# Kernel optimization log

Measured on AMD Instinct MI355X. Metric: run time of the kernel, lower is better.

Reference implementation:

```python
import jax, jax.numpy as jnp
import numpy as np

B, S, D, N, K = 2, 2048, 512, 32768, 64
CHUNK = 2048  # min(2048, num_slots) as in the torch source
EPS = 1e-8


def _phase_linear(x, Wr, Wi, br, bi):
    # complex linear on [..., d, 2] phase tensors
    xr, xi = x[..., 0], x[..., 1]
    yr = xr @ Wr.T - xi @ Wi.T + br
    yi = xr @ Wi.T + xi @ Wr.T + bi
    return jnp.stack([yr, yi], axis=-1)


def _phase_norm(x, gamma):
    # RMS normalization of the complex magnitude over dim, scaled by gamma
    mag2 = (x * x).sum(-1)                      # [..., d]
    rms = jnp.sqrt(mag2.mean(-1, keepdims=True) + EPS)
    return x * (gamma / rms)[..., None]


def setup_inputs() -> dict:
    key = jax.random.key(0)
    ks = jax.random.split(key, 8)
    inp = {
        'query': jax.random.normal(ks[0], (B, S, D, 2), jnp.float32),
        'keys': jax.random.normal(ks[1], (N, D, 2), jnp.float32) * 0.02,
        'values': jax.random.normal(ks[2], (N, D, 2), jnp.float32) * 0.02,
        'Wq_r': jax.random.normal(ks[3], (D, D), jnp.float32) * 0.02,
        'Wq_i': jax.random.normal(ks[4], (D, D), jnp.float32) * 0.02,
        'bq_r': jnp.zeros((D,), jnp.float32),
        'bq_i': jnp.zeros((D,), jnp.float32),
        'Wo_r': jax.random.normal(ks[5], (D, D), jnp.float32) * 0.02,
        'Wo_i': jax.random.normal(ks[6], (D, D), jnp.float32) * 0.02,
        'bo_r': jnp.zeros((D,), jnp.float32),
        'bo_i': jnp.zeros((D,), jnp.float32),
        'ln_gamma': jnp.ones((D,), jnp.float32),
        'top_k': K,
    }
    return inp


def _read(query, keys, values, Wq_r, Wq_i, bq_r, bq_i, Wo_r, Wo_i, bo_r, bo_i, ln_gamma, top_k):
    b, s, d, _ = query.shape
    n = keys.shape[0]
    q = _phase_linear(query, Wq_r, Wq_i, bq_r, bq_i)
    qf = q.reshape(b * s, d, 2)
    q_r, q_i = qf[..., 0], qf[..., 1]
    q_mag = jnp.sqrt((q_r * q_r + q_i * q_i).sum(-1) + EPS)  # [Q]
    nq = b * s

    n_chunks = n // CHUNK
    key_chunks = keys.reshape(n_chunks, CHUNK, d, 2)
    offsets = jnp.arange(n_chunks, dtype=jnp.int32) * CHUNK
    local_idx = jnp.arange(CHUNK, dtype=jnp.int32)

    def body(carry, xs):
        tv, ti = carry                      # [Q, K], [Q, K]
        ck, off = xs                        # [C, d, 2], scalar
        k_r, k_i = ck[..., 0], ck[..., 1]
        k_mag = jnp.sqrt((k_r * k_r + k_i * k_i).sum(-1) + EPS)   # [C]
        coh = q_r @ k_r.T + q_i @ k_i.T                            # [Q, C]
        coh = coh / (q_mag[:, None] * k_mag[None, :] + EPS)
        idx = jnp.broadcast_to(off + local_idx, (nq, CHUNK))
        cv = jnp.concatenate([tv, coh], axis=-1)
        ci = jnp.concatenate([ti, idx], axis=-1)
        nv, loc = jax.lax.top_k(cv, top_k)
        ni = jnp.take_along_axis(ci, loc, axis=-1)
        return (nv, ni), None

    init = (jnp.full((nq, top_k), -jnp.inf, jnp.float32),
            jnp.zeros((nq, top_k), jnp.int32))
    (topk_vals, topk_idx), _ = jax.lax.scan(body, init, (key_chunks, offsets))

    attn = jax.nn.softmax(topk_vals, axis=-1)                      # [Q, K]
    gathered = values[topk_idx]                                    # [Q, K, d, 2]
    retrieved = jnp.einsum('qk,qkdp->qdp', attn, gathered).reshape(b, s, d, 2)

    out = _phase_norm(retrieved, ln_gamma)
    out = _phase_linear(out, Wo_r, Wo_i, bo_r, bo_i)
    return out


def reference(query, keys, values, Wq_r, Wq_i, bq_r, bq_i, Wo_r, Wo_i, bo_r, bo_i, ln_gamma, top_k):
    return _read(query, keys, values, Wq_r, Wq_i, bq_r, bq_i, Wo_r, Wo_i, bo_r, bo_i, ln_gamma, top_k)
```

## Files before the change

### kernel.cpp

```cpp
#include <hip/hip_runtime.h>
#include <math.h>
#include <float.h>

#define EPSF 1e-8f
#define EPSD 1e-8
#define D_DIM 512
#define T_DIM 1024
#define K_TOP 64
#define K_KEEP 128
#define NBIN 2048
#define CAND_SORT 1024

typedef __bf16 bf16_t;
typedef __bf16 bf16x8 __attribute__((ext_vector_type(8)));
typedef __bf16 bf16x4 __attribute__((ext_vector_type(4)));
typedef float f32x4 __attribute__((ext_vector_type(4)));

__global__ __launch_bounds__(256)
void rownorm_convert_q_kernel(const double* __restrict__ X, double* __restrict__ magd,
                              bf16_t* __restrict__ Qn, int rows) {
  int r = blockIdx.x;
  if (r >= rows) return;
  int tid = threadIdx.x;
  const double* xr = X + (size_t)r * T_DIM;
  double v[4];
  double s = 0.0;
  #pragma unroll
  for (int i = 0; i < 4; i++) { v[i] = xr[tid * 4 + i]; s += v[i] * v[i]; }
  for (int o = 32; o > 0; o >>= 1) s += __shfl_down(s, o, 64);
  __shared__ double red[4];
  __shared__ double mag_s;
  if ((tid & 63) == 0) red[tid >> 6] = s;
  __syncthreads();
  if (tid == 0) {
    double m = sqrt(red[0] + red[1] + red[2] + red[3] + EPSD);
    magd[r] = m; mag_s = m;
  }
  __syncthreads();
  double inv = 1.0 / mag_s;
  bf16x4 o;
  #pragma unroll
  for (int i = 0; i < 4; i++) o[i] = (bf16_t)((float)(v[i] * inv));
  *(bf16x4*)(Qn + (size_t)r * T_DIM + tid * 4) = o;
}

__global__ __launch_bounds__(256)
void rownorm_convert_k_kernel(const float* __restrict__ X, double* __restrict__ magd,
                              bf16_t* __restrict__ Kn, int rows) {
  int r = blockIdx.x;
  if (r >= rows) return;
  int tid = threadIdx.x;
  float4 v = ((const float4*)(X + (size_t)r * T_DIM))[tid];
  double s = (double)v.x * v.x + (double)v.y * v.y + (double)v.z * v.z + (double)v.w * v.w;
  for (int o = 32; o > 0; o >>= 1) s += __shfl_down(s, o, 64);
  __shared__ double red[4];
  __shared__ float inv_s;
  if ((tid & 63) == 0) red[tid >> 6] = s;
  __syncthreads();
  if (tid == 0) {
    double m = sqrt(red[0] + red[1] + red[2] + red[3] + EPSD);
    magd[r] = m; inv_s = (float)(1.0 / m);
  }
  __syncthreads();
  float inv = inv_s;
  bf16x4 o;
  o[0] = (bf16_t)(v.x * inv); o[1] = (bf16_t)(v.y * inv);
  o[2] = (bf16_t)(v.z * inv); o[3] = (bf16_t)(v.w * inv);
  *(bf16x4*)(Kn + (size_t)r * T_DIM + tid * 4) = o;
}

__global__ __launch_bounds__(256)
void cgemm_f64_kernel(const float* __restrict__ X,
                      const float* __restrict__ Wr, const float* __restrict__ Wi,
                      const float* __restrict__ br, const float* __restrict__ bi,
                      double* __restrict__ Yd, int M) {
  __shared__ float Ar[16][64], Ai[16][64], Br_[16][64], Bi_[16][64];
  int tid = threadIdx.x;
  int tx = tid & 15, ty = tid >> 4;
  int m0 = blockIdx.x * 64, n0 = blockIdx.y * 64;
  double accR[4][4] = {{0}}, accI[4][4] = {{0}};
  for (int k0 = 0; k0 < D_DIM; k0 += 16) {
    #pragma unroll
    for (int gi = 0; gi < 2; gi++) {
      int g = tid + gi * 256;
      int m = g >> 3, dg = g & 7;
      float4 v = *(const float4*)(X + (size_t)(m0 + m) * T_DIM + 2 * k0 + dg * 4);
      Ar[dg*2][m] = v.x; Ai[dg*2][m] = v.y; Ar[dg*2+1][m] = v.z; Ai[dg*2+1][m] = v.w;
    }
    {
      int j = tid >> 2, c = tid & 3;
      float4 vr = *(const float4*)(Wr + (size_t)(n0 + j) * D_DIM + k0 + c * 4);
      float4 vi = *(const float4*)(Wi + (size_t)(n0 + j) * D_DIM + k0 + c * 4);
      Br_[c*4+0][j] = vr.x; Br_[c*4+1][j] = vr.y; Br_[c*4+2][j] = vr.z; Br_[c*4+3][j] = vr.w;
      Bi_[c*4+0][j] = vi.x; Bi_[c*4+1][j] = vi.y; Bi_[c*4+2][j] = vi.z; Bi_[c*4+3][j] = vi.w;
    }
    __syncthreads();
    #pragma unroll
    for (int k = 0; k < 16; k++) {
      float arr[4], aii[4], wrr[4], wii[4];
      *(float4*)arr = *(const float4*)&Ar[k][ty*4];
      *(float4*)aii = *(const float4*)&Ai[k][ty*4];
      *(float4*)wrr = *(const float4*)&Br_[k][tx*4];
      *(float4*)wii = *(const float4*)&Bi_[k][tx*4];
      #pragma unroll
      for (int im = 0; im < 4; im++)
        #pragma unroll
        for (int jn = 0; jn < 4; jn++) {
          double ar = (double)arr[im], ai = (double)aii[im];
          double wr = (double)wrr[jn], wi = (double)wii[jn];
          accR[im][jn] += ar * wr - ai * wi;
          accI[im][jn] += ar * wi + ai * wr;
        }
    }
    __syncthreads();
  }
  #pragma unroll
  for (int im = 0; im < 4; im++) {
    int m = m0 + ty * 4 + im;
    #pragma unroll
    for (int jn = 0; jn < 4; jn++) {
      int j = n0 + tx * 4 + jn;
      size_t base = (size_t)m * T_DIM + j * 2;
      Yd[base]     = accR[im][jn] + (double)br[j];
      Yd[base + 1] = accI[im][jn] + (double)bi[j];
    }
  }
}

__global__ __launch_bounds__(256)
void cgemm_kernel(const float* __restrict__ X,
                  const float* __restrict__ Wr, const float* __restrict__ Wi,
                  const float* __restrict__ br, const float* __restrict__ bi,
                  float* __restrict__ Y, int M) {
  __shared__ float Ar[16][64], Ai[16][64], Br_[16][64], Bi_[16][64];
  int tid = threadIdx.x;
  int tx = tid & 15, ty = tid >> 4;
  int m0 = blockIdx.x * 64, n0 = blockIdx.y * 64;
  float accR[4][4] = {{0}}, accI[4][4] = {{0}};
  for (int k0 = 0; k0 < D_DIM; k0 += 16) {
    #pragma unroll
    for (int gi = 0; gi < 2; gi++) {
      int g = tid + gi * 256;
      int m = g >> 3, dg = g & 7;
      float4 v = *(const float4*)(X + (size_t)(m0 + m) * T_DIM + 2 * k0 + dg * 4);
      Ar[dg*2][m] = v.x; Ai[dg*2][m] = v.y; Ar[dg*2+1][m] = v.z; Ai[dg*2+1][m] = v.w;
    }
    {
      int j = tid >> 2, c = tid & 3;
      float4 vr = *(const float4*)(Wr + (size_t)(n0 + j) * D_DIM + k0 + c * 4);
      float4 vi = *(const float4*)(Wi + (size_t)(n0 + j) * D_DIM + k0 + c * 4);
      Br_[c*4+0][j] = vr.x; Br_[c*4+1][j] = vr.y; Br_[c*4+2][j] = vr.z; Br_[c*4+3][j] = vr.w;
      Bi_[c*4+0][j] = vi.x; Bi_[c*4+1][j] = vi.y; Bi_[c*4+2][j] = vi.z; Bi_[c*4+3][j] = vi.w;
    }
    __syncthreads();
    #pragma unroll
    for (int k = 0; k < 16; k++) {
      float arr[4], aii[4], wrr[4], wii[4];
      *(float4*)arr = *(const float4*)&Ar[k][ty*4];
      *(float4*)aii = *(const float4*)&Ai[k][ty*4];
      *(float4*)wrr = *(const float4*)&Br_[k][tx*4];
      *(float4*)wii = *(const float4*)&Bi_[k][tx*4];
      #pragma unroll
      for (int im = 0; im < 4; im++)
        #pragma unroll
        for (int jn = 0; jn < 4; jn++) {
          accR[im][jn] += arr[im] * wrr[jn] - aii[im] * wii[jn];
          accI[im][jn] += arr[im] * wii[jn] + aii[im] * wrr[jn];
        }
    }
    __syncthreads();
  }
  #pragma unroll
  for (int im = 0; im < 4; im++) {
    int m = m0 + ty * 4 + im;
    #pragma unroll
    for (int jn = 0; jn < 4; jn++) {
      int j = n0 + tx * 4 + jn;
      float2 o; o.x = accR[im][jn] + br[j]; o.y = accI[im][jn] + bi[j];
      *(float2*)(Y + (size_t)m * T_DIM + j * 2) = o;
    }
  }
}

__global__ __launch_bounds__(256)
void mfma_score_kernel(const bf16_t* __restrict__ Qn, const bf16_t* __restrict__ Kn,
                       bf16_t* __restrict__ S, int n_off, int C) {
  __shared__ bf16_t As[128 * 32];
  __shared__ bf16_t Bs[128 * 32];
  __shared__ bf16_t Cs[128 * 128];
  int tid = threadIdx.x;
  int lane = tid & 63, wv = tid >> 6;
  int nwg = gridDim.x * gridDim.y;
  int wg = blockIdx.x + blockIdx.y * gridDim.x;
  int q8 = nwg >> 3, r8 = nwg & 7;
  int xcd = wg & 7, sub = wg >> 3;
  int swz = (xcd < r8 ? xcd * (q8 + 1) : r8 * (q8 + 1) + (xcd - r8) * q8) + sub;
  int mt = swz % gridDim.x, nt = swz / gridDim.x;
  int m0 = mt * 128;
  int n0 = nt * 128;
  int wm = (wv & 1) * 64, wn = (wv >> 1) * 64;
  f32x4 acc[4][4] = {};
  const bf16_t* Ag = Qn + (size_t)m0 * T_DIM;
  const bf16_t* Bg = Kn + (size_t)(n_off + n0) * T_DIM;
  int frow = lane & 15;
  int fk = (lane >> 4) * 8;
  for (int k0 = 0; k0 < T_DIM; k0 += 32) {
    #pragma unroll
    for (int it = 0; it < 2; it++) {
      int rbase = (it * 4 + wv) * 16;
      int row = rbase + (lane >> 2);
      int gcol = lane & 3;
      const bf16_t* gpa = Ag + (size_t)row * T_DIM + k0 + gcol * 8;
      const bf16_t* gpb = Bg + (size_t)row * T_DIM + k0 + gcol * 8;
      bf16_t* lpa = As + rbase * 32 + lane * 8;
      bf16_t* lpb = Bs + rbase * 32 + lane * 8;
      __builtin_amdgcn_global_load_lds(
          (const __attribute__((address_space(1))) void*)gpa,
          (__attribute__((address_space(3))) void*)lpa, 16, 0, 0);
      __builtin_amdgcn_global_load_lds(
          (const __attribute__((address_space(1))) void*)gpb,
          (__attribute__((address_space(3))) void*)lpb, 16, 0, 0);
    }
    __syncthreads();
    bf16x8 a[4], b[4];
    #pragma unroll
    for (int i = 0; i < 4; i++)
      a[i] = *(const bf16x8*)(As + (wm + i * 16 + frow) * 32 + fk);
    #pragma unroll
    for (int j = 0; j < 4; j++)
      b[j] = *(const bf16x8*)(Bs + (wn + j * 16 + frow) * 32 + fk);
    #pragma unroll
    for (int i = 0; i < 4; i++)
      #pragma unroll
      for (int j = 0; j < 4; j++)
        acc[i][j] = __builtin_amdgcn_mfma_f32_16x16x32_bf16(a[i], b[j], acc[i][j], 0, 0, 0);
    __syncthreads();
  }
  int col = lane & 15, qr = (lane >> 4) * 4;
  #pragma unroll
  for (int i = 0; i < 4; i++)
    #pragma unroll
    for (int j = 0; j < 4; j++)
      #pragma unroll
      for (int r = 0; r < 4; r++)
        Cs[(wm + i * 16 + qr + r) * 128 + (wn + j * 16 + col)] = (bf16_t)acc[i][j][r];
  __syncthreads();
  const float4* cs4 = (const float4*)Cs;
  #pragma unroll
  for (int it = 0; it < 8; it++) {
    int idx = it * 256 + tid;
    int row = idx >> 4;
    int cb  = idx & 15;
    *(float4*)((char*)S + ((size_t)(m0 + row) * C + n0) * 2 + cb * 16) = cs4[idx];
  }
}

__global__ __launch_bounds__(256)
void select_kernel(const bf16_t* __restrict__ S, int C, int key_off,
                   float* __restrict__ cand_v, int* __restrict__ cand_i,
                   int slot_off, int nslot) {
  int q = blockIdx.x, tid = threadIdx.x;
  __shared__ unsigned hist[NBIN];
  __shared__ unsigned psum[256];
  __shared__ unsigned redmax[4];
  __shared__ float bv[CAND_SORT];
  __shared__ int bi[CAND_SORT];
  __shared__ unsigned thr_s, cnt_s;
  const bf16x8* row8 = (const bf16x8*)(S + (size_t)q * C);
  int nvec = C >> 3;

  unsigned kmax = 0;
  for (int v = tid; v < nvec; v += 256) {
    bf16x8 x = row8[v];
    #pragma unroll
    for (int i = 0; i < 8; i++) {
      unsigned t = __float_as_uint((float)x[i]);
      t = (t & 0x80000000u) ? ~t : (t | 0x80000000u);
      unsigned k = t >> 16;
      kmax = kmax > k ? kmax : k;
    }
  }
  for (int o = 32; o > 0; o >>= 1) {
    unsigned other = (unsigned)__shfl_down((int)kmax, o, 64);
    kmax = kmax > other ? kmax : other;
  }
  if ((tid & 63) == 0) redmax[tid >> 6] = kmax;
  __syncthreads();
  unsigned rm01 = redmax[0] > redmax[1] ? redmax[0] : redmax[1];
  unsigned rm23 = redmax[2] > redmax[3] ? redmax[2] : redmax[3];
  unsigned rowmax = rm01 > rm23 ? rm01 : rm23;

  unsigned base = rowmax >= (unsigned)(NBIN - 1) ? rowmax - (unsigned)(NBIN - 1) : 0u;
  unsigned cntAbove = 0;
  unsigned thr = 0;
  while (true) {
    for (int i = tid; i < NBIN; i += 256) hist[i] = 0;
    __syncthreads();
    for (int v = tid; v < nvec; v += 256) {
      bf16x8 x = row8[v];
      #pragma unroll
      for (int i = 0; i < 8; i++) {
        unsigned t = __float_as_uint((float)x[i]);
        t = (t & 0x80000000u) ? ~t : (t | 0x80000000u);
        unsigned d = (t >> 16) - base;
        if (d < (unsigned)NBIN) atomicAdd(&hist[d], 1u);
      }
    }
    __syncthreads();
    unsigned sg = 0;
    #pragma unroll
    for (int b = 0; b < 8; b++) sg += hist[tid * 8 + b];
    psum[tid] = sg;
    __syncthreads();
    for (int off = 1; off < 256; off <<= 1) {
      unsigned v0 = psum[tid];
      unsigned ad = (tid + off < 256) ? psum[tid + off] : 0u;
      __syncthreads();
      psum[tid] = v0 + ad;
      __syncthreads();
    }
    unsigned K2 = (unsigned)K_KEEP - cntAbove;
    unsigned total = psum[0];
    if (total >= K2) {
      if (psum[tid] >= K2 && (tid == 255 || psum[tid + 1] < K2)) {
        unsigned acc = (tid == 255) ? 0u : psum[tid + 1];
        for (int b = tid * 8 + 7; b >= tid * 8; b--) {
          acc += hist[b];
          if (acc >= K2) { thr_s = base + (unsigned)b; break; }
        }
      }
      __syncthreads();
      thr = thr_s;
      break;
    }
    cntAbove += total;
    if (base == 0) { thr = 0; break; }
    base = base >= (unsigned)NBIN ? base - (unsigned)NBIN : 0u;
    __syncthreads();
  }

  if (tid == 0) cnt_s = 0;
  __syncthreads();
  for (int v = tid; v < nvec; v += 256) {
    bf16x8 x = row8[v];
    #pragma unroll
    for (int i = 0; i < 8; i++) {
      float fx = (float)x[i];
      unsigned t = __float_as_uint(fx);
      t = (t & 0x80000000u) ? ~t : (t | 0x80000000u);
      if ((t >> 16) >= thr) {
        unsigned p = atomicAdd(&cnt_s, 1u);
        if (p < (unsigned)CAND_SORT) { bv[p] = fx; bi[p] = key_off + v * 8 + i; }
      }
    }
  }
  __syncthreads();
  int cnt = (int)min(cnt_s, (unsigned)CAND_SORT);
  int n = K_KEEP; while (n < cnt) n <<= 1;
  for (int x = cnt + tid; x < n; x += 256) { bv[x] = -FLT_MAX; bi[x] = 0x7FFFFFFF; }
  for (int k = 2; k <= n; k <<= 1) {
    for (int j = k >> 1; j > 0; j >>= 1) {
      __syncthreads();
      for (int i = tid; i < n; i += 256) {
        int ixj = i ^ j;
        if (ixj > i) {
          float a = bv[i], b = bv[ixj];
          int ia = bi[i], ib = bi[ixj];
          bool a_worse = (a < b) || (a == b && ia > ib);
          bool up = ((i & k) == 0);
          if (up ? a_worse : !a_worse) {
            bv[i] = b; bv[ixj] = a; bi[i] = ib; bi[ixj] = ia;
          }
        }
      }
    }
  }
  __syncthreads();
  if (tid < K_KEEP) {
    cand_v[(size_t)q * nslot + slot_off + tid] = bv[tid];
    cand_i[(size_t)q * nslot + slot_off + tid] = bi[tid];
  }
}

__global__ __launch_bounds__(256)
void merge_kernel(const float* __restrict__ cand_v, const int* __restrict__ cand_i,
                  int nslot, int* __restrict__ topi) {
  int q = blockIdx.x, tid = threadIdx.x;
  __shared__ float bv[NBIN];
  __shared__ int bi[NBIN];
  int n = K_KEEP; while (n < nslot) n <<= 1;
  for (int i = tid; i < n; i += 256) {
    if (i < nslot) { bv[i] = cand_v[(size_t)q * nslot + i]; bi[i] = cand_i[(size_t)q * nslot + i]; }
    else { bv[i] = -FLT_MAX; bi[i] = 0x7FFFFFFF; }
  }
  for (int k = 2; k <= n; k <<= 1) {
    for (int j = k >> 1; j > 0; j >>= 1) {
      __syncthreads();
      for (int i = tid; i < n; i += 256) {
        int ixj = i ^ j;
        if (ixj > i) {
          float a = bv[i], b = bv[ixj];
          int ia = bi[i], ib = bi[ixj];
          bool a_worse = (a < b) || (a == b && ia > ib);
          bool up = ((i & k) == 0);
          if (up ? a_worse : !a_worse) {
            bv[i] = b; bv[ixj] = a; bi[i] = ib; bi[ixj] = ia;
          }
        }
      }
    }
  }
  __syncthreads();
  if (tid < K_KEEP) topi[q * K_KEEP + tid] = bi[tid];
}

__global__ __launch_bounds__(256)
void rescore_kernel(const int* __restrict__ topi,
                    const double* __restrict__ Qd,
                    const double* __restrict__ qmagd, const double* __restrict__ kmagd,
                    const float* __restrict__ Kk, const float* __restrict__ V,
                    const float* __restrict__ gamma,
                    float* __restrict__ XN) {
  int q = blockIdx.x, tid = threadIdx.x;
  __shared__ double qrow[T_DIM];
  __shared__ double cval[K_KEEP];
  __shared__ int cidx[K_KEEP];
  __shared__ float w[K_TOP];
  __shared__ int widx[K_TOP];
  __shared__ float red[4];
  for (int i = tid; i < T_DIM / 2; i += 256)
    ((double2*)qrow)[i] = ((const double2*)(Qd + (size_t)q * T_DIM))[i];
  if (tid < K_KEEP) cidx[tid] = topi[q * K_KEEP + tid];
  __syncthreads();
  double qm = qmagd[q];
  int wv = tid >> 6, ln = tid & 63;
  for (int c = wv; c < K_KEEP; c += 8) {
    int keyA = cidx[c];
    int keyB = cidx[c + 4];
    const float4* A4 = (const float4*)(Kk + (size_t)keyA * T_DIM);
    const float4* B4 = (const float4*)(Kk + (size_t)keyB * T_DIM);
    double sA = 0.0, sB = 0.0;
    #pragma unroll
    for (int it = 0; it < 4; it++) {
      float4 va = A4[ln + it * 64];
      float4 vb = B4[ln + it * 64];
      int t = (ln + it * 64) * 4;
      double q0 = qrow[t], q1 = qrow[t + 1], q2 = qrow[t + 2], q3 = qrow[t + 3];
      sA += (double)va.x * q0 + (double)va.y * q1 + (double)va.z * q2 + (double)va.w * q3;
      sB += (double)vb.x * q0 + (double)vb.y * q1 + (double)vb.z * q2 + (double)vb.w * q3;
    }
    for (int o = 32; o > 0; o >>= 1) {
      sA += __shfl_down(sA, o, 64);
      sB += __shfl_down(sB, o, 64);
    }
    if (ln == 0) {
      cval[c]     = sA / (qm * kmagd[keyA] + EPSD);
      cval[c + 4] = sB / (qm * kmagd[keyB] + EPSD);
    }
  }
  __syncthreads();
  for (int k = 2; k <= K_KEEP; k <<= 1) {
    for (int j = k >> 1; j > 0; j >>= 1) {
      __syncthreads();
      if (tid < K_KEEP) {
        int i = tid, ixj = i ^ j;
        if (ixj > i) {
          double a = cval[i], b = cval[ixj];
          int ia = cidx[i], ib = cidx[ixj];
          bool a_worse = (a < b) || (a == b && ia > ib);
          bool up = ((i & k) == 0);
          if (up ? a_worse : !a_worse) {
            cval[i] = b; cval[ixj] = a; cidx[i] = ib; cidx[ixj] = ia;
          }
        }
      }
    }
  }
  __syncthreads();
  if (tid < 64) {
    double v = cval[tid];
    double m = cval[0];
    double e = exp(v - m);
    double s = e;
    for (int o = 32; o > 0; o >>= 1) s += __shfl_down(s, o, 64);
    s = __shfl(s, 0, 64);
    w[tid] = (float)(e / s);
    widx[tid] = cidx[tid];
  }
  __syncthreads();
  float4 acc = {0.f, 0.f, 0.f, 0.f};
  #pragma unroll 8
  for (int j2 = 0; j2 < 64; j2++) {
    float wj = w[j2];
    float4 v = *(const float4*)(V + (size_t)widx[j2] * T_DIM + tid * 4);
    acc.x += wj * v.x; acc.y += wj * v.y; acc.z += wj * v.z; acc.w += wj * v.w;
  }
  float ls = acc.x*acc.x + acc.y*acc.y + acc.z*acc.z + acc.w*acc.w;
  for (int o = 32; o > 0; o >>= 1) ls += __shfl_down(ls, o, 64);
  if ((tid & 63) == 0) red[tid >> 6] = ls;
  __syncthreads();
  float tot = red[0] + red[1] + red[2] + red[3];
  float rms = sqrtf(tot / (float)D_DIM + EPSF);
  float g0 = gamma[tid * 2] / rms, g1 = gamma[tid * 2 + 1] / rms;
  float4 o = { acc.x * g0, acc.y * g0, acc.z * g1, acc.w * g1 };
  *(float4*)(XN + (size_t)q * T_DIM + tid * 4) = o;
}

extern "C" void kernel_launch(void* const* d_in, const int* in_sizes, int n_in,
                              void* d_out, int out_size, void* d_ws, size_t ws_size,
                              hipStream_t stream) {
  const float* query  = (const float*)d_in[0];
  const float* keys   = (const float*)d_in[1];
  const float* values = (const float*)d_in[2];
  const float* Wq_r   = (const float*)d_in[3];
  const float* Wq_i   = (const float*)d_in[4];
  const float* bq_r   = (const float*)d_in[5];
  const float* bq_i   = (const float*)d_in[6];
  const float* Wo_r   = (const float*)d_in[7];
  const float* Wo_i   = (const float*)d_in[8];
  const float* bo_r   = (const float*)d_in[9];
  const float* bo_i   = (const float*)d_in[10];
  const float* gamma  = (const float*)d_in[11];
  float* out = (float*)d_out;

  int M = in_sizes[0] / T_DIM;
  int N = in_sizes[1] / T_DIM;

  char* ws = (char*)d_ws;
  size_t off = 0;
  double* qd    = (double*)(ws + off); off += (size_t)M * T_DIM * 8;
  float*  xn    = (float*) (ws + off); off += (size_t)M * T_DIM * 4;
  double* qmagd = (double*)(ws + off); off += (size_t)M * 8;
  double* kmagd = (double*)(ws + off); off += (size_t)N * 8;
  int*    topi  = (int*)   (ws + off); off += (size_t)M * K_KEEP * 4;
  bf16_t* qn    = (bf16_t*)(ws + off); off += (size_t)M * T_DIM * 2;
  bf16_t* kn    = (bf16_t*)(ws + off); off += (size_t)N * T_DIM * 2;

  int C = 2048;
  for (int c = N; c >= 2048; c >>= 1) {
    size_t need = off + (size_t)M * c * 2
                + 2 * (size_t)M * (size_t)(N / c) * K_KEEP * 4;
    if (need <= ws_size) { C = c; break; }
  }
  if (C > N) C = N;
  int nchunks = N / C;
  int nslot = nchunks * K_KEEP;

  bf16_t* sc    = (bf16_t*)(ws + off); off += (size_t)M * C * 2;
  float*  candv = (float*) (ws + off); off += (size_t)M * nslot * 4;
  int*    candi = (int*)   (ws + off); off += (size_t)M * nslot * 4;

  dim3 blk(256);
  cgemm_f64_kernel<<<dim3(M / 64, D_DIM / 64), blk, 0, stream>>>(query, Wq_r, Wq_i, bq_r, bq_i, qd, M);
  rownorm_convert_q_kernel<<<dim3(M), blk, 0, stream>>>(qd, qmagd, qn, M);
  rownorm_convert_k_kernel<<<dim3(N), blk, 0, stream>>>(keys, kmagd, kn, N);
  for (int c = 0; c < nchunks; c++) {
    int noff = c * C;
    mfma_score_kernel<<<dim3(M / 128, C / 128), blk, 0, stream>>>(qn, kn, sc, noff, C);
    select_kernel<<<dim3(M), blk, 0, stream>>>(sc, C, noff, candv, candi, c * K_KEEP, nslot);
  }
  const int* top_src = candi;
  if (nchunks > 1) {
    merge_kernel<<<dim3(M), blk, 0, stream>>>(candv, candi, nslot, topi);
    top_src = topi;
  }
  rescore_kernel<<<dim3(M), blk, 0, stream>>>(top_src, qd, qmagd, kmagd, keys, values, gamma, xn);
  cgemm_kernel<<<dim3(M / 64, D_DIM / 64), blk, 0, stream>>>(xn, Wo_r, Wo_i, bo_r, bo_i, out, M);
}
```

Measured before the change: 1.826 ms.

## Compute per-row score max in GEMM epilogue and split rescore into two kernels

The score GEMM epilogue now reduces each row's max of the order-preserving bf16 keys and publishes it through a global atomicMax. This lets the select kernel skip its first full pass over the score row. The rowmax buffer is cleared only once, in the query normalisation kernel, so with several chunks it holds a running max across chunks rather than a per-chunk max. That could shift the histogram window for later chunks. Separately, the rescore kernel is split into a scoring/softmax kernel and a value gather-plus-norm kernel, with weights and indices passed through global memory, which adds a launch and a small round trip.

```diff
diff --git a/kernel.cpp b/kernel.cpp
--- a/kernel.cpp
+++ b/kernel.cpp
@@ -18,7 +18,8 @@
 
 __global__ __launch_bounds__(256)
 void rownorm_convert_q_kernel(const double* __restrict__ X, double* __restrict__ magd,
-                              bf16_t* __restrict__ Qn, int rows) {
+                              bf16_t* __restrict__ Qn, unsigned* __restrict__ rowmax,
+                              int rows) {
   int r = blockIdx.x;
   if (r >= rows) return;
   int tid = threadIdx.x;
@@ -35,6 +36,7 @@
   if (tid == 0) {
     double m = sqrt(red[0] + red[1] + red[2] + red[3] + EPSD);
     magd[r] = m; mag_s = m;
+    rowmax[r] = 0u;
   }
   __syncthreads();
   double inv = 1.0 / mag_s;
@@ -184,7 +186,8 @@
 
 __global__ __launch_bounds__(256)
 void mfma_score_kernel(const bf16_t* __restrict__ Qn, const bf16_t* __restrict__ Kn,
-                       bf16_t* __restrict__ S, int n_off, int C) {
+                       bf16_t* __restrict__ S, unsigned* __restrict__ rowmax,
+                       int n_off, int C) {
   __shared__ bf16_t As[128 * 32];
   __shared__ bf16_t Bs[128 * 32];
   __shared__ bf16_t Cs[128 * 128];
@@ -251,44 +254,40 @@
     int idx = it * 256 + tid;
     int row = idx >> 4;
     int cb  = idx & 15;
-    *(float4*)((char*)S + ((size_t)(m0 + row) * C + n0) * 2 + cb * 16) = cs4[idx];
+    float4 vv = cs4[idx];
+    *(float4*)((char*)S + ((size_t)(m0 + row) * C + n0) * 2 + cb * 16) = vv;
+    const unsigned short* us = (const unsigned short*)&vv;
+    unsigned km = 0;
+    #pragma unroll
+    for (int j = 0; j < 8; j++) {
+      unsigned u = us[j];
+      unsigned k16 = (u & 0x8000u) ? (~u & 0xFFFFu) : (u | 0x8000u);
+      km = km > k16 ? km : k16;
+    }
+    #pragma unroll
+    for (int msk = 1; msk < 16; msk <<= 1) {
+      unsigned other = (unsigned)__shfl_xor((int)km, msk, 64);
+      km = km > other ? km : other;
+    }
+    if ((tid & 15) == 0) atomicMax(&rowmax[m0 + row], km);
   }
 }
 
 __global__ __launch_bounds__(256)
 void select_kernel(const bf16_t* __restrict__ S, int C, int key_off,
+                   const unsigned* __restrict__ rowmax_g,
                    float* __restrict__ cand_v, int* __restrict__ cand_i,
                    int slot_off, int nslot) {
   int q = blockIdx.x, tid = threadIdx.x;
   __shared__ unsigned hist[NBIN];
   __shared__ unsigned psum[256];
-  __shared__ unsigned redmax[4];
   __shared__ float bv[CAND_SORT];
   __shared__ int bi[CAND_SORT];
   __shared__ unsigned thr_s, cnt_s;
   const bf16x8* row8 = (const bf16x8*)(S + (size_t)q * C);
   int nvec = C >> 3;
 
-  unsigned kmax = 0;
-  for (int v = tid; v < nvec; v += 256) {
-    bf16x8 x = row8[v];
-    #pragma unroll
-    for (int i = 0; i < 8; i++) {
-      unsigned t = __float_as_uint((float)x[i]);
-      t = (t & 0x80000000u) ? ~t : (t | 0x80000000u);
-      unsigned k = t >> 16;
-      kmax = kmax > k ? kmax : k;
-    }
-  }
-  for (int o = 32; o > 0; o >>= 1) {
-    unsigned other = (unsigned)__shfl_down((int)kmax, o, 64);
-    kmax = kmax > other ? kmax : other;
-  }
-  if ((tid & 63) == 0) redmax[tid >> 6] = kmax;
-  __syncthreads();
-  unsigned rm01 = redmax[0] > redmax[1] ? redmax[0] : redmax[1];
-  unsigned rm23 = redmax[2] > redmax[3] ? redmax[2] : redmax[3];
-  unsigned rowmax = rm01 > rm23 ? rm01 : rm23;
+  unsigned rowmax = rowmax_g[q];
 
   unsigned base = rowmax >= (unsigned)(NBIN - 1) ? rowmax - (unsigned)(NBIN - 1) : 0u;
   unsigned cntAbove = 0;
@@ -415,19 +414,15 @@
 }
 
 __global__ __launch_bounds__(256)
-void rescore_kernel(const int* __restrict__ topi,
-                    const double* __restrict__ Qd,
-                    const double* __restrict__ qmagd, const double* __restrict__ kmagd,
-                    const float* __restrict__ Kk, const float* __restrict__ V,
-                    const float* __restrict__ gamma,
-                    float* __restrict__ XN) {
+void rescore_score_kernel(const int* __restrict__ topi,
+                          const double* __restrict__ Qd,
+                          const double* __restrict__ qmagd, const double* __restrict__ kmagd,
+                          const float* __restrict__ Kk,
+                          float* __restrict__ wgt, int* __restrict__ widx_g) {
   int q = blockIdx.x, tid = threadIdx.x;
   __shared__ double qrow[T_DIM];
   __shared__ double cval[K_KEEP];
   __shared__ int cidx[K_KEEP];
-  __shared__ float w[K_TOP];
-  __shared__ int widx[K_TOP];
-  __shared__ float red[4];
   for (int i = tid; i < T_DIM / 2; i += 256)
     ((double2*)qrow)[i] = ((const double2*)(Qd + (size_t)q * T_DIM))[i];
   if (tid < K_KEEP) cidx[tid] = topi[q * K_KEEP + tid];
@@ -484,9 +479,20 @@
     double s = e;
     for (int o = 32; o > 0; o >>= 1) s += __shfl_down(s, o, 64);
     s = __shfl(s, 0, 64);
-    w[tid] = (float)(e / s);
-    widx[tid] = cidx[tid];
-  }
+    wgt[q * K_TOP + tid] = (float)(e / s);
+    widx_g[q * K_TOP + tid] = cidx[tid];
+  }
+}
+
+__global__ __launch_bounds__(256)
+void gather_norm_kernel(const float* __restrict__ wgt, const int* __restrict__ widx_g,
+                        const float* __restrict__ V, const float* __restrict__ gamma,
+                        float* __restrict__ XN) {
+  int q = blockIdx.x, tid = threadIdx.x;
+  __shared__ float w[K_TOP];
+  __shared__ int widx[K_TOP];
+  __shared__ float red[4];
+  if (tid < K_TOP) { w[tid] = wgt[q * K_TOP + tid]; widx[tid] = widx_g[q * K_TOP + tid]; }
   __syncthreads();
   float4 acc = {0.f, 0.f, 0.f, 0.f};
   #pragma unroll 8
@@ -528,13 +534,16 @@
 
   char* ws = (char*)d_ws;
   size_t off = 0;
-  double* qd    = (double*)(ws + off); off += (size_t)M * T_DIM * 8;
-  float*  xn    = (float*) (ws + off); off += (size_t)M * T_DIM * 4;
-  double* qmagd = (double*)(ws + off); off += (size_t)M * 8;
-  double* kmagd = (double*)(ws + off); off += (size_t)N * 8;
-  int*    topi  = (int*)   (ws + off); off += (size_t)M * K_KEEP * 4;
-  bf16_t* qn    = (bf16_t*)(ws + off); off += (size_t)M * T_DIM * 2;
-  bf16_t* kn    = (bf16_t*)(ws + off); off += (size_t)N * T_DIM * 2;
+  double*   qd     = (double*)  (ws + off); off += (size_t)M * T_DIM * 8;
+  float*    xn     = (float*)   (ws + off); off += (size_t)M * T_DIM * 4;
+  double*   qmagd  = (double*)  (ws + off); off += (size_t)M * 8;
+  double*   kmagd  = (double*)  (ws + off); off += (size_t)N * 8;
+  unsigned* rowmax = (unsigned*)(ws + off); off += (size_t)M * 4;
+  int*      topi   = (int*)     (ws + off); off += (size_t)M * K_KEEP * 4;
+  float*    wgt    = (float*)   (ws + off); off += (size_t)M * K_TOP * 4;
+  int*      widxg  = (int*)     (ws + off); off += (size_t)M * K_TOP * 4;
+  bf16_t*   qn     = (bf16_t*)  (ws + off); off += (size_t)M * T_DIM * 2;
+  bf16_t*   kn     = (bf16_t*)  (ws + off); off += (size_t)N * T_DIM * 2;
 
   int C = 2048;
   for (int c = N; c >= 2048; c >>= 1) {
@@ -552,18 +561,19 @@
 
   dim3 blk(256);
   cgemm_f64_kernel<<<dim3(M / 64, D_DIM / 64), blk, 0, stream>>>(query, Wq_r, Wq_i, bq_r, bq_i, qd, M);
-  rownorm_convert_q_kernel<<<dim3(M), blk, 0, stream>>>(qd, qmagd, qn, M);
+  rownorm_convert_q_kernel<<<dim3(M), blk, 0, stream>>>(qd, qmagd, qn, rowmax, M);
   rownorm_convert_k_kernel<<<dim3(N), blk, 0, stream>>>(keys, kmagd, kn, N);
   for (int c = 0; c < nchunks; c++) {
     int noff = c * C;
-    mfma_score_kernel<<<dim3(M / 128, C / 128), blk, 0, stream>>>(qn, kn, sc, noff, C);
-    select_kernel<<<dim3(M), blk, 0, stream>>>(sc, C, noff, candv, candi, c * K_KEEP, nslot);
+    mfma_score_kernel<<<dim3(M / 128, C / 128), blk, 0, stream>>>(qn, kn, sc, rowmax, noff, C);
+    select_kernel<<<dim3(M), blk, 0, stream>>>(sc, C, noff, rowmax, candv, candi, c * K_KEEP, nslot);
   }
   const int* top_src = candi;
   if (nchunks > 1) {
     merge_kernel<<<dim3(M), blk, 0, stream>>>(candv, candi, nslot, topi);
     top_src = topi;
   }
-  rescore_kernel<<<dim3(M), blk, 0, stream>>>(top_src, qd, qmagd, kmagd, keys, values, gamma, xn);
+  rescore_score_kernel<<<dim3(M), blk, 0, stream>>>(top_src, qd, qmagd, kmagd, keys, wgt, widxg);
+  gather_norm_kernel<<<dim3(M), blk, 0, stream>>>(wgt, widxg, values, gamma, xn);
   cgemm_kernel<<<dim3(M / 64, D_DIM / 64), blk, 0, stream>>>(xn, Wo_r, Wo_i, bo_r, bo_i, out, M);
 }
```

New measurement: 1.842 ms. No clear change (+0.9%).
